# Performance work log

Measured on AMD Instinct MI355X. Metric: run time of the kernel, lower is better.

Reference implementation:

```python
import jax, jax.numpy as jnp
import numpy as np

N_NODES = 50000
N_EDGES = 800000
D_FEAT = 64
UNITS = 128  # concat=True -> each kernel maps D_FEAT -> UNITS//2


def setup_inputs() -> dict:
    key = jax.random.key(0)
    k1, k2, k3, k4, k5 = jax.random.split(key, 5)
    x = jax.random.normal(k1, (N_NODES, D_FEAT), dtype=jnp.float32)
    edge_index = jax.random.randint(k2, (2, N_EDGES), 0, N_NODES, dtype=jnp.int64)
    edge_weight = jax.random.uniform(k3, (N_EDGES,), dtype=jnp.float32)
    glorot = np.sqrt(6.0 / (D_FEAT + UNITS // 2)).astype(np.float32)
    self_kernel = jax.random.uniform(k4, (D_FEAT, UNITS // 2), dtype=jnp.float32, minval=-glorot, maxval=glorot)
    neighbor_kernel = jax.random.uniform(k5, (D_FEAT, UNITS // 2), dtype=jnp.float32, minval=-glorot, maxval=glorot)
    bias = jnp.zeros((UNITS,), dtype=jnp.float32)
    return {"x": x, "edge_index": edge_index, "edge_weight": edge_weight,
            "self_kernel": self_kernel, "neighbor_kernel": neighbor_kernel, "bias": bias}


def reference(x, edge_index, edge_weight, self_kernel, neighbor_kernel, bias):
    num_nodes = x.shape[0]
    row, col = edge_index[0], edge_index[1]  # row: target node, col: source neighbor
    # gather neighbor features and apply edge weights
    neighbor_x = x[col] * edge_weight[:, None]  # [E, D]
    # segment-mean over incoming edges of each target node
    sums = jax.ops.segment_sum(neighbor_x, row, num_segments=num_nodes)  # [N, D]
    counts = jax.ops.segment_sum(jnp.ones_like(edge_weight), row, num_segments=num_nodes)  # [N]
    neighbor_mean = sums / jnp.maximum(counts, 1.0)[:, None]
    # dual projection + concat (concat=True)
    from_self = x @ self_kernel              # [N, UNITS//2]
    from_neigh = neighbor_mean @ neighbor_kernel  # [N, UNITS//2]
    h = jnp.concatenate([from_self, from_neigh], axis=1) + bias
    h = jax.nn.relu(h)
    # normalize=False -> no l2 normalize
    return h
```

## Files before the change

### kernel.cpp

```cpp
#include <hip/hip_runtime.h>


typedef unsigned long long ull;
typedef __attribute__((ext_vector_type(8))) short bf16x8;
typedef __attribute__((ext_vector_type(4))) float f32x4;

constexpr int N_NODES = 50000;
constexpr int N_EDGES = 800000;
constexpr int D = 64;
constexpr int UNITS = 128;
constexpr int NB = (N_NODES + 255) / 256;
constexpr int SC_EPT = 16;
constexpr int SC_THREADS = 256;
constexpr int SC_CHUNK = SC_EPT * SC_THREADS;
constexpr int SC_BLOCKS = (N_EDGES + SC_CHUNK - 1) / SC_CHUNK;
constexpr int NS_THREADS = 256;
constexpr int NS_EPT = 24;
constexpr int PREP_BLOCKS = 2048;
constexpr int NTILES = N_NODES / 16;
constexpr int PJ_BLOCKS = (NTILES + 3) / 4;

__device__ __forceinline__ unsigned f2bf(float f) {
    unsigned u = __float_as_uint(f);
    return (u + 0x7fffu + ((u >> 16) & 1u)) >> 16;
}
__device__ __forceinline__ float bf2f(unsigned b) {
    return __uint_as_float(b << 16);
}

__global__ __launch_bounds__(256) void prep(const float* __restrict__ x,
                                            unsigned* __restrict__ xh,
                                            const int* __restrict__ ei,
                                            int* __restrict__ partial) {
    constexpr int XW = N_NODES * (D / 2);
    for (int i = blockIdx.x * 256 + threadIdx.x; i < XW; i += PREP_BLOCKS * 256) {
        const float2 v = ((const float2*)x)[i];
        xh[i] = f2bf(v.x) | (f2bf(v.y) << 16);
    }
    if (blockIdx.x < SC_BLOCKS) {
        __shared__ int lh[NB];
        for (int i = threadIdx.x; i < NB; i += 256) lh[i] = 0;
        __syncthreads();
        const int e0 = blockIdx.x * SC_CHUNK + threadIdx.x;
        #pragma unroll
        for (int i = 0; i < SC_EPT; ++i) {
            int e = e0 + i * SC_THREADS;
            if (e < N_EDGES) atomicAdd(&lh[ei[e] >> 8], 1);
        }
        __syncthreads();
        int* row = partial + (size_t)blockIdx.x * NB;
        for (int i = threadIdx.x; i < NB; i += 256) row[i] = lh[i];
    }
}

__global__ __launch_bounds__(256) void scan_cols(int* __restrict__ partial,
                                                 int* __restrict__ btot) {
    __shared__ int s[256];
    const int b = blockIdx.x;
    const int t = threadIdx.x;
    const int v = (t < SC_BLOCKS) ? partial[(size_t)t * NB + b] : 0;
    s[t] = v;
    __syncthreads();
    for (int d2 = 1; d2 < 256; d2 <<= 1) {
        int u = (t >= d2) ? s[t - d2] : 0;
        __syncthreads();
        s[t] += u;
        __syncthreads();
    }
    if (t < SC_BLOCKS) partial[(size_t)t * NB + b] = s[t] - v;
    if (t == 255) btot[b] = s[255];
}

__global__ __launch_bounds__(SC_THREADS) void edge_scatter(const int* __restrict__ ei,
                                                           const float* __restrict__ ew,
                                                           const int* __restrict__ partial,
                                                           const int* __restrict__ btot,
                                                           ull* __restrict__ packed) {
    __shared__ int sb[256];
    __shared__ int lbase[NB];
    __shared__ int lcur[NB];
    const int t = threadIdx.x;
    const int bv = (t < NB) ? btot[t] : 0;
    sb[t] = bv;
    __syncthreads();
    for (int d2 = 1; d2 < 256; d2 <<= 1) {
        int u = (t >= d2) ? sb[t - d2] : 0;
        __syncthreads();
        sb[t] += u;
        __syncthreads();
    }
    const int* row = partial + (size_t)blockIdx.x * NB;
    if (t < NB) {
        lbase[t] = (sb[t] - bv) + row[t];
        lcur[t]  = 0;
    }
    __syncthreads();
    const int e0 = blockIdx.x * SC_CHUNK + t;
    #pragma unroll
    for (int i = 0; i < SC_EPT; ++i) {
        const int e = e0 + i * SC_THREADS;
        if (e < N_EDGES) {
            const int   r = ei[e];
            const int   c = ei[N_EDGES + e];
            const float w = ew[e];
            const int   b = r >> 8;
            const int   lpos = atomicAdd(&lcur[b], 1);
            const unsigned hi = (unsigned)c | ((unsigned)(r & 255) << 16);
            packed[lbase[b] + lpos] = ((ull)hi << 32) | (ull)(unsigned)__float_as_uint(w);
        }
    }
}

__global__ __launch_bounds__(NS_THREADS) void node_sort(const int* __restrict__ btot,
                                                        int* __restrict__ offs,
                                                        const ull* __restrict__ packed,
                                                        unsigned* __restrict__ cedges) {
    __shared__ int cur[256];
    __shared__ int sc[256];
    __shared__ int sBase, sEnd;
    const int b = blockIdx.x;
    const int t = threadIdx.x;

    const int bv = (t < NB) ? btot[t] : 0;
    sc[t] = bv;
    __syncthreads();
    for (int d2 = 1; d2 < 256; d2 <<= 1) {
        int u = (t >= d2) ? sc[t - d2] : 0;
        __syncthreads();
        sc[t] += u;
        __syncthreads();
    }
    if (t == b) { sBase = sc[t] - bv; sEnd = sc[t]; }
    __syncthreads();
    const int s = sBase;
    const int e = sEnd;

    ull st[NS_EPT];
    #pragma unroll
    for (int i = 0; i < NS_EPT; ++i) {
        const int idx = s + t + i * NS_THREADS;
        st[i] = (idx < e) ? packed[idx] : ~0ull;
    }
    cur[t] = 0;
    __syncthreads();
    #pragma unroll
    for (int i = 0; i < NS_EPT; ++i) {
        if (st[i] != ~0ull) atomicAdd(&cur[(int)((st[i] >> 48) & 0xff)], 1);
    }
    __syncthreads();
    const int v = cur[t];
    sc[t] = v;
    __syncthreads();
    for (int d2 = 1; d2 < 256; d2 <<= 1) {
        int u = (t >= d2) ? sc[t - d2] : 0;
        __syncthreads();
        sc[t] += u;
        __syncthreads();
    }
    const int excl = sc[t] - v;
    const int n = b * 256 + t;
    if (n < N_NODES) offs[n] = s + excl;
    if (b == 0 && t == 0) offs[N_NODES] = N_EDGES;
    cur[t] = excl;
    __syncthreads();
    #pragma unroll
    for (int i = 0; i < NS_EPT; ++i) {
        if (st[i] != ~0ull) {
            const int r8  = (int)((st[i] >> 48) & 0xff);
            const int pos = atomicAdd(&cur[r8], 1);
            const unsigned hi  = (unsigned)(st[i] >> 32);
            const unsigned col = hi & 0xffffu;
            const unsigned wbf = f2bf(__uint_as_float((unsigned)st[i]));
            cedges[s + pos] = (col << 16) | wbf;
        }
    }
}

__global__ __launch_bounds__(256) void sage_aggregate(const unsigned* __restrict__ xh,
                                                      const int* __restrict__ offs,
                                                      const unsigned* __restrict__ cedges,
                                                      unsigned* __restrict__ meanh) {
    const int n = (blockIdx.x * 256 + threadIdx.x) >> 5;
    if (n >= N_NODES) return;
    const int fp = threadIdx.x & 31;
    const int s = offs[n];
    const int t = offs[n + 1];

    float a0x = 0.f, a0y = 0.f, a1x = 0.f, a1y = 0.f;
    float a2x = 0.f, a2y = 0.f, a3x = 0.f, a3y = 0.f;
    float a4x = 0.f, a4y = 0.f, a5x = 0.f, a5y = 0.f;
    float a6x = 0.f, a6y = 0.f, a7x = 0.f, a7y = 0.f;
    int e = s;
    for (; e + 7 < t; e += 8) {
        const unsigned c0 = cedges[e],     c1 = cedges[e + 1];
        const unsigned c2 = cedges[e + 2], c3 = cedges[e + 3];
        const unsigned c4 = cedges[e + 4], c5 = cedges[e + 5];
        const unsigned c6 = cedges[e + 6], c7 = cedges[e + 7];
        const unsigned v0 = xh[(c0 >> 16) * (D / 2) + fp];
        const unsigned v1 = xh[(c1 >> 16) * (D / 2) + fp];
        const unsigned v2 = xh[(c2 >> 16) * (D / 2) + fp];
        const unsigned v3 = xh[(c3 >> 16) * (D / 2) + fp];
        const unsigned v4 = xh[(c4 >> 16) * (D / 2) + fp];
        const unsigned v5 = xh[(c5 >> 16) * (D / 2) + fp];
        const unsigned v6 = xh[(c6 >> 16) * (D / 2) + fp];
        const unsigned v7 = xh[(c7 >> 16) * (D / 2) + fp];
        const float w0 = bf2f(c0 & 0xffffu), w1 = bf2f(c1 & 0xffffu);
        const float w2 = bf2f(c2 & 0xffffu), w3 = bf2f(c3 & 0xffffu);
        const float w4 = bf2f(c4 & 0xffffu), w5 = bf2f(c5 & 0xffffu);
        const float w6 = bf2f(c6 & 0xffffu), w7 = bf2f(c7 & 0xffffu);
        a0x = fmaf(__uint_as_float(v0 << 16),         w0, a0x);
        a0y = fmaf(__uint_as_float(v0 & 0xffff0000u), w0, a0y);
        a1x = fmaf(__uint_as_float(v1 << 16),         w1, a1x);
        a1y = fmaf(__uint_as_float(v1 & 0xffff0000u), w1, a1y);
        a2x = fmaf(__uint_as_float(v2 << 16),         w2, a2x);
        a2y = fmaf(__uint_as_float(v2 & 0xffff0000u), w2, a2y);
        a3x = fmaf(__uint_as_float(v3 << 16),         w3, a3x);
        a3y = fmaf(__uint_as_float(v3 & 0xffff0000u), w3, a3y);
        a4x = fmaf(__uint_as_float(v4 << 16),         w4, a4x);
        a4y = fmaf(__uint_as_float(v4 & 0xffff0000u), w4, a4y);
        a5x = fmaf(__uint_as_float(v5 << 16),         w5, a5x);
        a5y = fmaf(__uint_as_float(v5 & 0xffff0000u), w5, a5y);
        a6x = fmaf(__uint_as_float(v6 << 16),         w6, a6x);
        a6y = fmaf(__uint_as_float(v6 & 0xffff0000u), w6, a6y);
        a7x = fmaf(__uint_as_float(v7 << 16),         w7, a7x);
        a7y = fmaf(__uint_as_float(v7 & 0xffff0000u), w7, a7y);
    }
    for (; e + 3 < t; e += 4) {
        const unsigned c0 = cedges[e],     c1 = cedges[e + 1];
        const unsigned c2 = cedges[e + 2], c3 = cedges[e + 3];
        const unsigned v0 = xh[(c0 >> 16) * (D / 2) + fp];
        const unsigned v1 = xh[(c1 >> 16) * (D / 2) + fp];
        const unsigned v2 = xh[(c2 >> 16) * (D / 2) + fp];
        const unsigned v3 = xh[(c3 >> 16) * (D / 2) + fp];
        const float w0 = bf2f(c0 & 0xffffu), w1 = bf2f(c1 & 0xffffu);
        const float w2 = bf2f(c2 & 0xffffu), w3 = bf2f(c3 & 0xffffu);
        a0x = fmaf(__uint_as_float(v0 << 16),         w0, a0x);
        a0y = fmaf(__uint_as_float(v0 & 0xffff0000u), w0, a0y);
        a1x = fmaf(__uint_as_float(v1 << 16),         w1, a1x);
        a1y = fmaf(__uint_as_float(v1 & 0xffff0000u), w1, a1y);
        a2x = fmaf(__uint_as_float(v2 << 16),         w2, a2x);
        a2y = fmaf(__uint_as_float(v2 & 0xffff0000u), w2, a2y);
        a3x = fmaf(__uint_as_float(v3 << 16),         w3, a3x);
        a3y = fmaf(__uint_as_float(v3 & 0xffff0000u), w3, a3y);
    }
    for (; e < t; ++e) {
        const unsigned c = cedges[e];
        const unsigned v = xh[(c >> 16) * (D / 2) + fp];
        const float w = bf2f(c & 0xffffu);
        a0x = fmaf(__uint_as_float(v << 16),         w, a0x);
        a0y = fmaf(__uint_as_float(v & 0xffff0000u), w, a0y);
    }
    const float inv = 1.0f / fmaxf((float)(t - s), 1.0f);
    const float mx = (((a0x + a1x) + (a2x + a3x)) + ((a4x + a5x) + (a6x + a7x))) * inv;
    const float my = (((a0y + a1y) + (a2y + a3y)) + ((a4y + a5y) + (a6y + a7y))) * inv;
    meanh[n * (D / 2) + fp] = f2bf(mx) | (f2bf(my) << 16);
}

__global__ __launch_bounds__(256) void sage_project(const unsigned* __restrict__ xh,
                                                    const unsigned* __restrict__ meanh,
                                                    const float* __restrict__ skern,
                                                    const float* __restrict__ nkern,
                                                    const float* __restrict__ bias,
                                                    float* __restrict__ out) {
    const int lane = threadIdx.x & 63;
    const int wid  = (blockIdx.x * 256 + threadIdx.x) >> 6;
    const int r16  = lane & 15;
    const int g    = lane >> 4;

    bf16x8 bfrag[16];
    #pragma unroll
    for (int ct = 0; ct < 8; ++ct) {
        const float* K = (ct < 4) ? skern : nkern;
        const int col = (ct & 3) * 16 + r16;
        #pragma unroll
        for (int kh = 0; kh < 2; ++kh) {
            bf16x8 f;
            #pragma unroll
            for (int j = 0; j < 8; ++j) {
                const int k = kh * 32 + 8 * g + j;
                f[j] = (short)f2bf(K[k * 64 + col]);
            }
            bfrag[ct * 2 + kh] = f;
        }
    }

    if (wid >= NTILES) return;
    const int n0 = wid * 16;

    const unsigned* xrow = xh    + (size_t)(n0 + r16) * (D / 2);
    const unsigned* mrow = meanh + (size_t)(n0 + r16) * (D / 2);
    const bf16x8 aS0 = *(const bf16x8*)(xrow + 4 * g);
    const bf16x8 aS1 = *(const bf16x8*)(xrow + 16 + 4 * g);
    const bf16x8 aN0 = *(const bf16x8*)(mrow + 4 * g);
    const bf16x8 aN1 = *(const bf16x8*)(mrow + 16 + 4 * g);

    f32x4 acc[8];
    #pragma unroll
    for (int ct = 0; ct < 8; ++ct) {
        f32x4 c = {0.f, 0.f, 0.f, 0.f};
        c = __builtin_amdgcn_mfma_f32_16x16x32_bf16(ct < 4 ? aS0 : aN0, bfrag[ct * 2 + 0], c, 0, 0, 0);
        c = __builtin_amdgcn_mfma_f32_16x16x32_bf16(ct < 4 ? aS1 : aN1, bfrag[ct * 2 + 1], c, 0, 0, 0);
        acc[ct] = c;
    }

    #pragma unroll
    for (int ct = 0; ct < 8; ++ct) {
        const int col = (ct < 4 ? 0 : 64) + (ct & 3) * 16 + r16;
        const float bj = bias[col];
        #pragma unroll
        for (int r = 0; r < 4; ++r) {
            const int node = n0 + 4 * g + r;
            out[(size_t)node * UNITS + col] = fmaxf(acc[ct][r] + bj, 0.0f);
        }
    }
}

extern "C" void kernel_launch(void* const* d_in, const int* in_sizes, int n_in,
                              void* d_out, int out_size, void* d_ws, size_t ws_size,
                              hipStream_t stream) {
    const float* x     = (const float*)d_in[0];
    const int*   ei    = (const int*)  d_in[1];
    const float* ew    = (const float*)d_in[2];
    const float* skern = (const float*)d_in[3];
    const float* nkern = (const float*)d_in[4];
    const float* bias  = (const float*)d_in[5];
    float* out = (float*)d_out;

    auto align256 = [](size_t v) { return (v + 255) & ~size_t(255); };
    const size_t szM  = align256((size_t)SC_BLOCKS * NB * sizeof(int));
    const size_t szT  = align256((size_t)NB * sizeof(int));
    const size_t szNO = align256((size_t)(N_NODES + 1) * sizeof(int));
    const size_t szP  = align256((size_t)N_EDGES * sizeof(ull));
    const size_t szC  = align256((size_t)N_EDGES * sizeof(unsigned));
    const size_t szX  = align256((size_t)N_NODES * (D / 2) * sizeof(unsigned));

    char* w = (char*)d_ws;
    int*      partial = (int*)w;
    int*      btot    = (int*)(w + szM);
    int*      offs    = (int*)(w + szM + szT);
    ull*      packed  = (ull*)(w + szM + szT + szNO);
    unsigned* cedges  = (unsigned*)(w + szM + szT + szNO + szP);
    unsigned* xh      = (unsigned*)(w + szM + szT + szNO + szP + szC);
    unsigned* meanh   = (unsigned*)(w + szM + szT + szNO + szP + szC + szX);
    (void)ws_size; (void)in_sizes; (void)n_in; (void)out_size;

    prep          <<<PREP_BLOCKS, 256, 0, stream>>>(x, xh, ei, partial);
    scan_cols     <<<NB, 256, 0, stream>>>(partial, btot);
    edge_scatter  <<<SC_BLOCKS, SC_THREADS, 0, stream>>>(ei, ew, partial, btot, packed);
    node_sort     <<<NB, NS_THREADS, 0, stream>>>(btot, offs, packed, cedges);
    sage_aggregate<<<(N_NODES * 32 + 255) / 256, 256, 0, stream>>>(xh, offs, cedges, meanh);
    sage_project  <<<PJ_BLOCKS, 256, 0, stream>>>(xh, meanh, skern, nkern, bias, out);
}
```

Baseline: 67.83 us.

## Split aggregation edges across lane groups with 16-byte vector gathers

```diff
diff --git a/kernel.cpp b/kernel.cpp
--- a/kernel.cpp
+++ b/kernel.cpp
@@ -182,78 +182,68 @@
                                                       unsigned* __restrict__ meanh) {
     const int n = (blockIdx.x * 256 + threadIdx.x) >> 5;
     if (n >= N_NODES) return;
-    const int fp = threadIdx.x & 31;
+    const int l32 = threadIdx.x & 31;
+    const int eg  = l32 >> 3;
+    const int wq  = l32 & 7;
     const int s = offs[n];
     const int t = offs[n + 1];
 
-    float a0x = 0.f, a0y = 0.f, a1x = 0.f, a1y = 0.f;
-    float a2x = 0.f, a2y = 0.f, a3x = 0.f, a3y = 0.f;
-    float a4x = 0.f, a4y = 0.f, a5x = 0.f, a5y = 0.f;
-    float a6x = 0.f, a6y = 0.f, a7x = 0.f, a7y = 0.f;
-    int e = s;
-    for (; e + 7 < t; e += 8) {
-        const unsigned c0 = cedges[e],     c1 = cedges[e + 1];
-        const unsigned c2 = cedges[e + 2], c3 = cedges[e + 3];
-        const unsigned c4 = cedges[e + 4], c5 = cedges[e + 5];
-        const unsigned c6 = cedges[e + 6], c7 = cedges[e + 7];
-        const unsigned v0 = xh[(c0 >> 16) * (D / 2) + fp];
-        const unsigned v1 = xh[(c1 >> 16) * (D / 2) + fp];
-        const unsigned v2 = xh[(c2 >> 16) * (D / 2) + fp];
-        const unsigned v3 = xh[(c3 >> 16) * (D / 2) + fp];
-        const unsigned v4 = xh[(c4 >> 16) * (D / 2) + fp];
-        const unsigned v5 = xh[(c5 >> 16) * (D / 2) + fp];
-        const unsigned v6 = xh[(c6 >> 16) * (D / 2) + fp];
-        const unsigned v7 = xh[(c7 >> 16) * (D / 2) + fp];
-        const float w0 = bf2f(c0 & 0xffffu), w1 = bf2f(c1 & 0xffffu);
-        const float w2 = bf2f(c2 & 0xffffu), w3 = bf2f(c3 & 0xffffu);
-        const float w4 = bf2f(c4 & 0xffffu), w5 = bf2f(c5 & 0xffffu);
-        const float w6 = bf2f(c6 & 0xffffu), w7 = bf2f(c7 & 0xffffu);
-        a0x = fmaf(__uint_as_float(v0 << 16),         w0, a0x);
-        a0y = fmaf(__uint_as_float(v0 & 0xffff0000u), w0, a0y);
-        a1x = fmaf(__uint_as_float(v1 << 16),         w1, a1x);
-        a1y = fmaf(__uint_as_float(v1 & 0xffff0000u), w1, a1y);
-        a2x = fmaf(__uint_as_float(v2 << 16),         w2, a2x);
-        a2y = fmaf(__uint_as_float(v2 & 0xffff0000u), w2, a2y);
-        a3x = fmaf(__uint_as_float(v3 << 16),         w3, a3x);
-        a3y = fmaf(__uint_as_float(v3 & 0xffff0000u), w3, a3y);
-        a4x = fmaf(__uint_as_float(v4 << 16),         w4, a4x);
-        a4y = fmaf(__uint_as_float(v4 & 0xffff0000u), w4, a4y);
-        a5x = fmaf(__uint_as_float(v5 << 16),         w5, a5x);
-        a5y = fmaf(__uint_as_float(v5 & 0xffff0000u), w5, a5y);
-        a6x = fmaf(__uint_as_float(v6 << 16),         w6, a6x);
-        a6y = fmaf(__uint_as_float(v6 & 0xffff0000u), w6, a6y);
-        a7x = fmaf(__uint_as_float(v7 << 16),         w7, a7x);
-        a7y = fmaf(__uint_as_float(v7 & 0xffff0000u), w7, a7y);
-    }
-    for (; e + 3 < t; e += 4) {
-        const unsigned c0 = cedges[e],     c1 = cedges[e + 1];
-        const unsigned c2 = cedges[e + 2], c3 = cedges[e + 3];
-        const unsigned v0 = xh[(c0 >> 16) * (D / 2) + fp];
-        const unsigned v1 = xh[(c1 >> 16) * (D / 2) + fp];
-        const unsigned v2 = xh[(c2 >> 16) * (D / 2) + fp];
-        const unsigned v3 = xh[(c3 >> 16) * (D / 2) + fp];
-        const float w0 = bf2f(c0 & 0xffffu), w1 = bf2f(c1 & 0xffffu);
-        const float w2 = bf2f(c2 & 0xffffu), w3 = bf2f(c3 & 0xffffu);
-        a0x = fmaf(__uint_as_float(v0 << 16),         w0, a0x);
-        a0y = fmaf(__uint_as_float(v0 & 0xffff0000u), w0, a0y);
-        a1x = fmaf(__uint_as_float(v1 << 16),         w1, a1x);
-        a1y = fmaf(__uint_as_float(v1 & 0xffff0000u), w1, a1y);
-        a2x = fmaf(__uint_as_float(v2 << 16),         w2, a2x);
-        a2y = fmaf(__uint_as_float(v2 & 0xffff0000u), w2, a2y);
-        a3x = fmaf(__uint_as_float(v3 << 16),         w3, a3x);
-        a3y = fmaf(__uint_as_float(v3 & 0xffff0000u), w3, a3y);
-    }
-    for (; e < t; ++e) {
-        const unsigned c = cedges[e];
-        const unsigned v = xh[(c >> 16) * (D / 2) + fp];
-        const float w = bf2f(c & 0xffffu);
-        a0x = fmaf(__uint_as_float(v << 16),         w, a0x);
-        a0y = fmaf(__uint_as_float(v & 0xffff0000u), w, a0y);
-    }
-    const float inv = 1.0f / fmaxf((float)(t - s), 1.0f);
-    const float mx = (((a0x + a1x) + (a2x + a3x)) + ((a4x + a5x) + (a6x + a7x))) * inv;
-    const float my = (((a0y + a1y) + (a2y + a3y)) + ((a4y + a5y) + (a6y + a7y))) * inv;
-    meanh[n * (D / 2) + fp] = f2bf(mx) | (f2bf(my) << 16);
+    float ax0 = 0.f, ay0 = 0.f, ax1 = 0.f, ay1 = 0.f;
+    float ax2 = 0.f, ay2 = 0.f, ax3 = 0.f, ay3 = 0.f;
+    float bx0 = 0.f, by0 = 0.f, bx1 = 0.f, by1 = 0.f;
+    float bx2 = 0.f, by2 = 0.f, bx3 = 0.f, by3 = 0.f;
+
+    if (t > s) {
+        const int tm1 = t - 1;
+        for (int g = s; g < t; g += 8) {
+            const int eA = g + eg;
+            const int eB = g + 4 + eg;
+            const unsigned cA = cedges[min(eA, tm1)];
+            const unsigned cB = cedges[min(eB, tm1)];
+            const float wA = (eA < t) ? bf2f(cA & 0xffffu) : 0.0f;
+            const float wB = (eB < t) ? bf2f(cB & 0xffffu) : 0.0f;
+            const uint4 vA = *(const uint4*)(xh + (size_t)(cA >> 16) * (D / 2) + wq * 4);
+            const uint4 vB = *(const uint4*)(xh + (size_t)(cB >> 16) * (D / 2) + wq * 4);
+            ax0 = fmaf(__uint_as_float(vA.x << 16),         wA, ax0);
+            ay0 = fmaf(__uint_as_float(vA.x & 0xffff0000u), wA, ay0);
+            ax1 = fmaf(__uint_as_float(vA.y << 16),         wA, ax1);
+            ay1 = fmaf(__uint_as_float(vA.y & 0xffff0000u), wA, ay1);
+            ax2 = fmaf(__uint_as_float(vA.z << 16),         wA, ax2);
+            ay2 = fmaf(__uint_as_float(vA.z & 0xffff0000u), wA, ay2);
+            ax3 = fmaf(__uint_as_float(vA.w << 16),         wA, ax3);
+            ay3 = fmaf(__uint_as_float(vA.w & 0xffff0000u), wA, ay3);
+            bx0 = fmaf(__uint_as_float(vB.x << 16),         wB, bx0);
+            by0 = fmaf(__uint_as_float(vB.x & 0xffff0000u), wB, by0);
+            bx1 = fmaf(__uint_as_float(vB.y << 16),         wB, bx1);
+            by1 = fmaf(__uint_as_float(vB.y & 0xffff0000u), wB, by1);
+            bx2 = fmaf(__uint_as_float(vB.z << 16),         wB, bx2);
+            by2 = fmaf(__uint_as_float(vB.z & 0xffff0000u), wB, by2);
+            bx3 = fmaf(__uint_as_float(vB.w << 16),         wB, bx3);
+            by3 = fmaf(__uint_as_float(vB.w & 0xffff0000u), wB, by3);
+        }
+    }
+    float sx0 = ax0 + bx0, sy0 = ay0 + by0;
+    float sx1 = ax1 + bx1, sy1 = ay1 + by1;
+    float sx2 = ax2 + bx2, sy2 = ay2 + by2;
+    float sx3 = ax3 + bx3, sy3 = ay3 + by3;
+    sx0 += __shfl_xor(sx0, 8);  sx0 += __shfl_xor(sx0, 16);
+    sy0 += __shfl_xor(sy0, 8);  sy0 += __shfl_xor(sy0, 16);
+    sx1 += __shfl_xor(sx1, 8);  sx1 += __shfl_xor(sx1, 16);
+    sy1 += __shfl_xor(sy1, 8);  sy1 += __shfl_xor(sy1, 16);
+    sx2 += __shfl_xor(sx2, 8);  sx2 += __shfl_xor(sx2, 16);
+    sy2 += __shfl_xor(sy2, 8);  sy2 += __shfl_xor(sy2, 16);
+    sx3 += __shfl_xor(sx3, 8);  sx3 += __shfl_xor(sx3, 16);
+    sy3 += __shfl_xor(sy3, 8);  sy3 += __shfl_xor(sy3, 16);
+
+    if (eg == 0) {
+        const float inv = 1.0f / fmaxf((float)(t - s), 1.0f);
+        uint4 r;
+        r.x = f2bf(sx0 * inv) | (f2bf(sy0 * inv) << 16);
+        r.y = f2bf(sx1 * inv) | (f2bf(sy1 * inv) << 16);
+        r.z = f2bf(sx2 * inv) | (f2bf(sy2 * inv) << 16);
+        r.w = f2bf(sx3 * inv) | (f2bf(sy3 * inv) << 16);
+        *(uint4*)(meanh + (size_t)n * (D / 2) + wq * 4) = r;
+    }
 }
 
 __global__ __launch_bounds__(256) void sage_project(const unsigned* __restrict__ xh,
```

After: 64.73 us. 1.05x faster.
